# Kernel tuning notes

Measured on AMD Instinct MI355X. Metric: run time of the kernel, lower is better.

The kernel has to match this reference:

```python
import jax, jax.numpy as jnp
import numpy as np


def setup_inputs() -> dict:
    key = jax.random.key(0)
    ks = jax.random.split(key, 6)
    B, C, H, W = 8, 128, 64, 64
    return {
        "curr_features": jax.random.normal(ks[0], (B, C, H, W), jnp.float32),
        "w1": jax.random.normal(ks[1], (C, 2 * C), jnp.float32) * 0.05,   # conv1x1 (2C->C)
        "b1": jnp.zeros((C,), jnp.float32),
        "gamma": jnp.ones((C,), jnp.float32),
        "beta": jnp.zeros((C,), jnp.float32),
        "running_mean": jax.random.normal(ks[2], (C,), jnp.float32) * 0.1,
        "running_var": jax.random.uniform(ks[3], (C,), jnp.float32, 0.5, 1.5),
        "w2": jax.random.normal(ks[4], (1, C), jnp.float32) * 0.05,       # conv1x1 (C->1)
        "b2": jnp.zeros((1,), jnp.float32),
    }


def reference(curr_features, w1, b1, gamma, beta, running_mean, running_var, w2, b2):
    B, C, H, W = curr_features.shape
    M = H * W
    BN_EPS = 1e-5
    LEAKY_SLOPE = 0.01  # InPlaceABNSync default activation: leaky_relu(0.01)

    f = curr_features.reshape(B, C, M)                       # [B,C,M]
    scores = jnp.einsum('bcm,bcn->bmn', f, f) * (C ** -0.5)  # [B,M,M]
    p = jax.nn.softmax(scores, axis=-1)
    feats1 = jnp.einsum('bmn,bcn->bcm', p, f)                # [B,C,M]

    x = jnp.concatenate([feats1, f], axis=1).reshape(B, 2 * C, H, W)

    # cls head: conv1x1 -> BN(inference) -> leaky_relu -> (dropout=identity in eval) -> conv1x1
    y = jnp.einsum('oc,bchw->bohw', w1, x) + b1[None, :, None, None]
    scale = gamma / jnp.sqrt(running_var + BN_EPS)
    y = (y - running_mean[None, :, None, None]) * scale[None, :, None, None] + beta[None, :, None, None]
    y = jnp.where(y >= 0, y, LEAKY_SLOPE * y)
    pred = jnp.einsum('oc,bchw->bohw', w2, y) + b2[None, :, None, None]  # [B,1,H,W]
    return pred
```

## Files before the change

kernel.cpp:

```cpp
#include <hip/hip_runtime.h>

#define NB 8
#define NC 128
#define NM 4096
#define FRAG 512

typedef __attribute__((ext_vector_type(8))) short short8;
typedef __attribute__((ext_vector_type(4))) float floatx4;

#define MFMA(a, b, c) __builtin_amdgcn_mfma_f32_16x16x32_bf16(a, b, c, 0, 0, 0)
#define EXP2F(x) __builtin_amdgcn_exp2f(x)

union S8U { short8 v; uint2 u2[2]; };

__device__ __forceinline__ unsigned pack2bf(float a, float b) {
    unsigned ua = __float_as_uint(a);
    unsigned ub = __float_as_uint(b);
    ua += 0x7fffu + ((ua >> 16) & 1u);
    ub += 0x7fffu + ((ub >> 16) & 1u);
    return (ua >> 16) | (ub & 0xffff0000u);
}

__device__ __forceinline__ unsigned cvt_pk_bf16(float a, float b) {
    unsigned r;
    asm("v_cvt_pk_bf16_f32 %0, %1, %2" : "=v"(r) : "v"(a), "v"(b));
    return r;
}

__constant__ float SF_C = 0.35712442f;
__constant__ float RS_C = 2.8001530f;


__global__ __launch_bounds__(256) void k_prep(
    const float* __restrict__ f, const float* __restrict__ w1,
    unsigned short* __restrict__ fX, unsigned short* __restrict__ gX)
{
    __shared__ __align__(16) char smem[50176];
    float (*Ls)[65] = (float (*)[65])smem;
    unsigned short (*LsT)[132] =
        (unsigned short (*)[132])(smem + 33280);
    unsigned short (*gt2)[72] = (unsigned short (*)[72])smem;

    const int tid   = threadIdx.x;
    const int b     = blockIdx.x & 7;
    const int chunk = blockIdx.x >> 3;
    const int m0    = chunk * 64;
    const float* fb = f + (size_t)b * NC * NM;
    #pragma unroll
    for (int k = 0; k < 32; ++k) {
        int idx = tid + k * 256;
        int c = idx >> 6, mm = idx & 63;
        Ls[c][mm] = fb[(size_t)c * NM + m0 + mm];
    }
    __syncthreads();

    const float sf = SF_C;
    const int m  = tid >> 2;
    const int ks = tid & 3;
    const int ch = ks * 32;
    unsigned pk[16];
    #pragma unroll
    for (int i = 0; i < 16; ++i)
        pk[i] = pack2bf(Ls[ch + 2 * i][m] * sf, Ls[ch + 2 * i + 1][m] * sf);
    {
        const int Mg  = m0 + m;
        const int mt  = Mg >> 4;
        const int lmm = Mg & 15;
        unsigned short* dst = fX + ((size_t)b * 256 + mt) * 4 * FRAG + ks * FRAG;
        #pragma unroll
        for (int q = 0; q < 4; ++q)
            *(uint4*)(dst + (q * 16 + lmm) * 8) =
                make_uint4(pk[4 * q], pk[4 * q + 1], pk[4 * q + 2], pk[4 * q + 3]);
    }
    #pragma unroll
    for (int q = 0; q < 4; ++q)
        *(uint4*)&LsT[m][ks * 32 + q * 8] =
            make_uint4(pk[4 * q], pk[4 * q + 1], pk[4 * q + 2], pk[4 * q + 3]);
    __syncthreads();

    const int wv = tid >> 6;
    const int l  = tid & 63;
    const int lm = l & 15;
    const int lq = l >> 4;
    const float rs = RS_C;

    short8 wf2[2][4];
    #pragma unroll
    for (int j = 0; j < 2; ++j) {
        const int o = (wv * 2 + j) * 16 + lm;
        #pragma unroll
        for (int kk = 0; kk < 4; ++kk) {
            const float* wp = w1 + (size_t)o * (2 * NC) + kk * 32 + lq * 8;
            S8U t;
            t.u2[0] = make_uint2(pack2bf(wp[0] * rs, wp[1] * rs),
                                 pack2bf(wp[2] * rs, wp[3] * rs));
            t.u2[1] = make_uint2(pack2bf(wp[4] * rs, wp[5] * rs),
                                 pack2bf(wp[6] * rs, wp[7] * rs));
            wf2[j][kk] = t.v;
        }
    }
    #pragma unroll
    for (int nt = 0; nt < 4; ++nt) {
        short8 af[4];
        #pragma unroll
        for (int kk = 0; kk < 4; ++kk)
            af[kk] = *(const short8*)&LsT[nt * 16 + lm][kk * 32 + lq * 8];
        #pragma unroll
        for (int j = 0; j < 2; ++j) {
            floatx4 D = {0.f, 0.f, 0.f, 0.f};
            #pragma unroll
            for (int kk = 0; kk < 4; ++kk)
                D = MFMA(af[kk], wf2[j][kk], D);
            *(uint2*)&gt2[(wv * 2 + j) * 16 + lm][nt * 16 + lq * 4] =
                make_uint2(pack2bf(D[0], D[1]), pack2bf(D[2], D[3]));
        }
    }
    __syncthreads();

    const int nblk = chunk >> 1;
    const int k2b  = (chunk & 1) * 2;
    #pragma unroll
    for (int j = 0; j < 2; ++j) {
        const int ot = wv * 2 + j;
        #pragma unroll
        for (int k2l = 0; k2l < 2; ++k2l) {
            uint4 v = *(const uint4*)&gt2[ot * 16 + lm][k2l * 32 + lq * 8];
            *(uint4*)(gX + (((size_t)b * 32 + nblk) * 8 + ot) * 4 * FRAG
                      + (k2b + k2l) * FRAG + l * 8) = v;
        }
    }
}

__global__ __launch_bounds__(256, 2) void k_attn(
    const unsigned short* __restrict__ fX,
    const unsigned short* __restrict__ gX,
    const float* __restrict__ w1,
    const float* __restrict__ b1v, const float* __restrict__ gammav,
    const float* __restrict__ betav, const float* __restrict__ rmeanv,
    const float* __restrict__ rvarv, const float* __restrict__ w2v,
    const float* __restrict__ b2v, float* __restrict__ out)
{
    __shared__ __align__(16) char Ps[2][16384];
    __shared__ float lpart[4][64];
    __shared__ float opart[4][64];

    const int tid = threadIdx.x;
    const int w   = tid >> 6;
    const int l   = tid & 63;
    const int lm  = l & 15;
    const int lq  = l >> 4;
    const int b   = blockIdx.x & 7;
    const int m0  = (blockIdx.x >> 3) * 64;

    const int lq0 = lq & 1;
    const int lq1 = lq >> 1;
    const int lm3 = lm >> 3;
    const unsigned Xsw = (unsigned)(((lq1 << 1) | lm3) << 4);
    const unsigned wofsA =
        ((((unsigned)(w >> 1) * 4 * 16) + ((unsigned)(2 * (w & 1) + lq1) * 16)
          + (unsigned)lm) * 16 + (unsigned)(8 * lq0)) ^ Xsw;
    const unsigned rofs = ((unsigned)l * 16) ^ ((((unsigned)l >> 3) & 3u) << 4);

    const unsigned short* fXb = fX + (size_t)b * NM * NC;
    const unsigned short* gXb = gX + (size_t)b * NC * NM;

    short8 qf[4][4];
    {
        const int qt0 = m0 >> 4;
        #pragma unroll
        for (int mt = 0; mt < 4; ++mt)
            #pragma unroll
            for (int ks = 0; ks < 4; ++ks)
                qf[mt][ks] = *(const short8*)
                    (fXb + (size_t)(qt0 + mt) * 4 * FRAG + ks * FRAG + l * 8);
    }

    const unsigned short* kpA = fXb + (size_t)w * 4 * FRAG + l * 8;
    const unsigned short* kpB = fXb + (size_t)(4 + w) * 4 * FRAG + l * 8;
    const unsigned short* gp0 = gXb + (size_t)(2 * w) * 4 * FRAG + l * 8;
    const unsigned short* gp1 = gXb + (size_t)(2 * w + 1) * 4 * FRAG + l * 8;

    short8 kfA[4], kfB[4];
    short8 gA0[4], gA1[4], gB0[4], gB1[4];
    #pragma unroll
    for (int ks = 0; ks < 4; ++ks) {
        kfA[ks] = *(const short8*)(kpA + ks * FRAG);
        kfB[ks] = *(const short8*)(kpB + ks * FRAG);
    }
    #pragma unroll
    for (int k2 = 0; k2 < 4; ++k2) {
        gA0[k2] = *(const short8*)(gp0 + k2 * FRAG);
        gA1[k2] = *(const short8*)(gp1 + k2 * FRAG);
    }

    floatx4 u[4][2];
    float lsum[4] = {0.f, 0.f, 0.f, 0.f};
    #pragma unroll
    for (int mt = 0; mt < 4; ++mt) {
        u[mt][0] = (floatx4){0.f, 0.f, 0.f, 0.f};
        u[mt][1] = (floatx4){0.f, 0.f, 0.f, 0.f};
    }

    {
        floatx4 svA[4], svB[4];
        __builtin_amdgcn_s_setprio(1);
        #pragma unroll
        for (int mt = 0; mt < 4; ++mt) {
            floatx4 a = {-24.f, -24.f, -24.f, -24.f};
            floatx4 bb = {-24.f, -24.f, -24.f, -24.f};
            #pragma unroll
            for (int ks = 0; ks < 4; ++ks) {
                a  = MFMA(kfA[ks], qf[mt][ks], a);
                bb = MFMA(kfB[ks], qf[mt][ks], bb);
            }
            svA[mt] = a; svB[mt] = bb;
        }
        __builtin_amdgcn_s_setprio(0);
        kpA += 8 * 4 * FRAG; kpB += 8 * 4 * FRAG;
        #pragma unroll
        for (int ks = 0; ks < 4; ++ks) {
            kfA[ks] = *(const short8*)(kpA + ks * FRAG);
            kfB[ks] = *(const short8*)(kpB + ks * FRAG);
        }
        char* psb = Ps[0];
        #pragma unroll
        for (int mt = 0; mt < 4; ++mt) {
            float pA0 = EXP2F(svA[mt][0]);
            float pA1 = EXP2F(svA[mt][1]);
            float pA2 = EXP2F(svA[mt][2]);
            float pA3 = EXP2F(svA[mt][3]);
            float pB0 = EXP2F(svB[mt][0]);
            float pB1 = EXP2F(svB[mt][1]);
            float pB2 = EXP2F(svB[mt][2]);
            float pB3 = EXP2F(svB[mt][3]);
            lsum[mt] += ((pA0 + pA1) + (pA2 + pA3)) +
                        ((pB0 + pB1) + (pB2 + pB3));
            *(uint2*)(psb + mt * 4096 + wofsA) =
                make_uint2(cvt_pk_bf16(pA0, pA1), cvt_pk_bf16(pA2, pA3));
            *(uint2*)(psb + mt * 4096 + wofsA + 2048) =
                make_uint2(cvt_pk_bf16(pB0, pB1), cvt_pk_bf16(pB2, pB3));
        }
        __syncthreads();
    }

    auto body = [&](char* psW, char* psR,
                    short8 (&gC0)[4], short8 (&gC1)[4],
                    short8 (&gN0)[4], short8 (&gN1)[4], bool loadK) {
        floatx4 svA[4], svB[4];
        __builtin_amdgcn_s_setprio(1);
        #pragma unroll
        for (int mt = 0; mt < 4; ++mt) {
            floatx4 a = {-24.f, -24.f, -24.f, -24.f};
            floatx4 bb = {-24.f, -24.f, -24.f, -24.f};
            #pragma unroll
            for (int ks = 0; ks < 4; ++ks) {
                a  = MFMA(kfA[ks], qf[mt][ks], a);
                bb = MFMA(kfB[ks], qf[mt][ks], bb);
            }
            svA[mt] = a; svB[mt] = bb;
        }
        __builtin_amdgcn_s_setprio(0);
        if (loadK) {
            kpA += 8 * 4 * FRAG; kpB += 8 * 4 * FRAG;
            #pragma unroll
            for (int ks = 0; ks < 4; ++ks) {
                kfA[ks] = *(const short8*)(kpA + ks * FRAG);
                kfB[ks] = *(const short8*)(kpB + ks * FRAG);
            }
        }
        gp0 += 8 * 4 * FRAG; gp1 += 8 * 4 * FRAG;
        #pragma unroll
        for (int k2 = 0; k2 < 4; ++k2) {
            gN0[k2] = *(const short8*)(gp0 + k2 * FRAG);
            gN1[k2] = *(const short8*)(gp1 + k2 * FRAG);
        }
        #pragma unroll
        for (int k2 = 0; k2 < 4; ++k2) {
            short8 pf[4];
            #pragma unroll
            for (int mt = 0; mt < 4; ++mt)
                pf[mt] = *(const short8*)(psR + mt * 4096 + k2 * 1024 + rofs);
            __builtin_amdgcn_s_setprio(1);
            #pragma unroll
            for (int mt = 0; mt < 4; ++mt) {
                u[mt][0] = MFMA(pf[mt], gC0[k2], u[mt][0]);
                u[mt][1] = MFMA(pf[mt], gC1[k2], u[mt][1]);
            }
            __builtin_amdgcn_s_setprio(0);
        }
        #pragma unroll
        for (int mt = 0; mt < 4; ++mt) {
            float pA0 = EXP2F(svA[mt][0]);
            float pA1 = EXP2F(svA[mt][1]);
            float pA2 = EXP2F(svA[mt][2]);
            float pA3 = EXP2F(svA[mt][3]);
            float pB0 = EXP2F(svB[mt][0]);
            float pB1 = EXP2F(svB[mt][1]);
            float pB2 = EXP2F(svB[mt][2]);
            float pB3 = EXP2F(svB[mt][3]);
            lsum[mt] += ((pA0 + pA1) + (pA2 + pA3)) +
                        ((pB0 + pB1) + (pB2 + pB3));
            *(uint2*)(psW + mt * 4096 + wofsA) =
                make_uint2(cvt_pk_bf16(pA0, pA1), cvt_pk_bf16(pA2, pA3));
            *(uint2*)(psW + mt * 4096 + wofsA + 2048) =
                make_uint2(cvt_pk_bf16(pB0, pB1), cvt_pk_bf16(pB2, pB3));
        }
        __syncthreads();
    };

    for (int i = 0; i < 15; ++i) {
        body(Ps[1], Ps[0], gA0, gA1, gB0, gB1, true);
        body(Ps[0], Ps[1], gB0, gB1, gA0, gA1, true);
    }
    body(Ps[1], Ps[0], gA0, gA1, gB0, gB1, false);

    #pragma unroll
    for (int k2 = 0; k2 < 4; ++k2) {
        short8 pf[4];
        #pragma unroll
        for (int mt = 0; mt < 4; ++mt)
            pf[mt] = *(const short8*)(Ps[1] + mt * 4096 + k2 * 1024 + rofs);
        __builtin_amdgcn_s_setprio(1);
        #pragma unroll
        for (int mt = 0; mt < 4; ++mt) {
            u[mt][0] = MFMA(pf[mt], gB0[k2], u[mt][0]);
            u[mt][1] = MFMA(pf[mt], gB1[k2], u[mt][1]);
        }
        __builtin_amdgcn_s_setprio(0);
    }

    #pragma unroll
    for (int mt = 0; mt < 4; ++mt) {
        lsum[mt] += __shfl_xor(lsum[mt], 16);
        lsum[mt] += __shfl_xor(lsum[mt], 32);
    }
    if (lq == 0) {
        #pragma unroll
        for (int mt = 0; mt < 4; ++mt)
            lpart[w][mt * 16 + lm] = lsum[mt];
    }

    floatx4 hacc[4][2];
    {
        const float rs = RS_C;
        #pragma unroll
        for (int j = 0; j < 2; ++j) {
            int o = w * 32 + j * 16 + lm;
            short8 wf[4];
            #pragma unroll
            for (int ks = 0; ks < 4; ++ks) {
                const float* wp = w1 + (size_t)o * (2 * NC) + NC + ks * 32 + lq * 8;
                S8U t;
                t.u2[0] = make_uint2(pack2bf(wp[0] * rs, wp[1] * rs),
                                     pack2bf(wp[2] * rs, wp[3] * rs));
                t.u2[1] = make_uint2(pack2bf(wp[4] * rs, wp[5] * rs),
                                     pack2bf(wp[6] * rs, wp[7] * rs));
                wf[ks] = t.v;
            }
            #pragma unroll
            for (int mt = 0; mt < 4; ++mt) {
                floatx4 a = {0.f, 0.f, 0.f, 0.f};
                #pragma unroll
                for (int ks = 0; ks < 4; ++ks)
                    a = MFMA(qf[mt][ks], wf[ks], a);
                hacc[mt][j] = a;
            }
        }
    }
    __syncthreads();

    float Abn[2], Dbn[2], W2[2];
    #pragma unroll
    for (int j = 0; j < 2; ++j) {
        int o = w * 32 + j * 16 + lm;
        float Ar = gammav[o] * rsqrtf(rvarv[o] + 1e-5f);
        Abn[j] = Ar;
        Dbn[j] = (b1v[o] - rmeanv[o]) * Ar + betav[o];
        W2[j]  = w2v[o];
    }
    float av[16];
    #pragma unroll
    for (int mt = 0; mt < 4; ++mt) {
        float4 L0 = *(const float4*)&lpart[0][mt * 16 + lq * 4];
        float4 L1 = *(const float4*)&lpart[1][mt * 16 + lq * 4];
        float4 L2 = *(const float4*)&lpart[2][mt * 16 + lq * 4];
        float4 L3 = *(const float4*)&lpart[3][mt * 16 + lq * 4];
        float4 Lt;
        Lt.x = (L0.x + L1.x) + (L2.x + L3.x);
        Lt.y = (L0.y + L1.y) + (L2.y + L3.y);
        Lt.z = (L0.z + L1.z) + (L2.z + L3.z);
        Lt.w = (L0.w + L1.w) + (L2.w + L3.w);
        #pragma unroll
        for (int r = 0; r < 4; ++r) {
            float rl = 1.f / ((const float*)&Lt)[r];
            float t0 = Abn[0] * (u[mt][0][r] * rl + hacc[mt][0][r]) + Dbn[0];
            float t1 = Abn[1] * (u[mt][1][r] * rl + hacc[mt][1][r]) + Dbn[1];
            t0 = t0 >= 0.f ? t0 : 0.01f * t0;
            t1 = t1 >= 0.f ? t1 : 0.01f * t1;
            av[mt * 4 + r] = W2[0] * t0 + W2[1] * t1;
        }
    }
    #pragma unroll
    for (int i = 0; i < 16; ++i) {
        av[i] += __shfl_xor(av[i], 1);
        av[i] += __shfl_xor(av[i], 2);
        av[i] += __shfl_xor(av[i], 4);
        av[i] += __shfl_xor(av[i], 8);
    }
    if (lm == 0) {
        #pragma unroll
        for (int mt = 0; mt < 4; ++mt)
            #pragma unroll
            for (int r = 0; r < 4; ++r)
                opart[w][mt * 16 + lq * 4 + r] = av[mt * 4 + r];
    }
    __syncthreads();
    if (tid < 64)
        out[(size_t)b * NM + m0 + tid] =
            b2v[0] + opart[0][tid] + opart[1][tid] + opart[2][tid] + opart[3][tid];
}

extern "C" void kernel_launch(void* const* d_in, const int* in_sizes, int n_in,
                              void* d_out, int out_size, void* d_ws, size_t ws_size,
                              hipStream_t stream) {
    const float* f     = (const float*)d_in[0];
    const float* w1    = (const float*)d_in[1];
    const float* b1    = (const float*)d_in[2];
    const float* gamma = (const float*)d_in[3];
    const float* beta  = (const float*)d_in[4];
    const float* rmean = (const float*)d_in[5];
    const float* rvar  = (const float*)d_in[6];
    const float* w2    = (const float*)d_in[7];
    const float* b2    = (const float*)d_in[8];
    float* out = (float*)d_out;

    unsigned short* fX = (unsigned short*)d_ws;
    unsigned short* gX = fX + (size_t)NB * NM * NC;

    hipLaunchKernelGGL(k_prep, dim3(512), dim3(256), 0, stream, f, w1, fX, gX);
    hipLaunchKernelGGL(k_attn, dim3(512), dim3(256), 0, stream,
                       fX, gX, w1, b1, gamma, beta, rmean, rvar, w2, b2, out);
}
```

Before: 159.8 us.

## Split attention over key halves with partial outputs and a merge kernel

Turns the fused attention kernel into a split-K (flash-decoding style) pair: k_attn_p processes half the key range per block across 1024 blocks with a higher occupancy bound, writing unnormalized partial outputs and row sums to workspace. A new k_merge kernel adds the two halves, normalizes, and applies the conv/BN/leaky/conv head. It also reorders the exp/LDS write ahead of the PV MFMA inside the loop body. The aim is more parallelism and occupancy on a 512-block grid; the cost is extra workspace traffic, a third launch, and a fallback path if workspace is too small.

```diff
diff --git a/kernel.cpp b/kernel.cpp
--- a/kernel.cpp
+++ b/kernel.cpp
@@ -29,7 +29,6 @@
 
 __constant__ float SF_C = 0.35712442f;
 __constant__ float RS_C = 2.8001530f;
-
 
 __global__ __launch_bounds__(256) void k_prep(
     const float* __restrict__ f, const float* __restrict__ w1,
@@ -131,26 +130,23 @@
     }
 }
 
-__global__ __launch_bounds__(256, 2) void k_attn(
+__global__ __launch_bounds__(256, 4) void k_attn_p(
     const unsigned short* __restrict__ fX,
     const unsigned short* __restrict__ gX,
-    const float* __restrict__ w1,
-    const float* __restrict__ b1v, const float* __restrict__ gammav,
-    const float* __restrict__ betav, const float* __restrict__ rmeanv,
-    const float* __restrict__ rvarv, const float* __restrict__ w2v,
-    const float* __restrict__ b2v, float* __restrict__ out)
+    float* __restrict__ uP, float* __restrict__ lP)
 {
     __shared__ __align__(16) char Ps[2][16384];
     __shared__ float lpart[4][64];
-    __shared__ float opart[4][64];
 
     const int tid = threadIdx.x;
     const int w   = tid >> 6;
     const int l   = tid & 63;
     const int lm  = l & 15;
     const int lq  = l >> 4;
-    const int b   = blockIdx.x & 7;
-    const int m0  = (blockIdx.x >> 3) * 64;
+    const int s   = blockIdx.x & 511;
+    const int b   = s & 7;
+    const int m0  = ((s >> 3) & 63) * 64;
+    const int nh  = blockIdx.x >> 9;
 
     const int lq0 = lq & 1;
     const int lq1 = lq >> 1;
@@ -175,10 +171,10 @@
                     (fXb + (size_t)(qt0 + mt) * 4 * FRAG + ks * FRAG + l * 8);
     }
 
-    const unsigned short* kpA = fXb + (size_t)w * 4 * FRAG + l * 8;
-    const unsigned short* kpB = fXb + (size_t)(4 + w) * 4 * FRAG + l * 8;
-    const unsigned short* gp0 = gXb + (size_t)(2 * w) * 4 * FRAG + l * 8;
-    const unsigned short* gp1 = gXb + (size_t)(2 * w + 1) * 4 * FRAG + l * 8;
+    const unsigned short* kpA = fXb + (size_t)(nh * 128 + w) * 4 * FRAG + l * 8;
+    const unsigned short* kpB = fXb + (size_t)(nh * 128 + 4 + w) * 4 * FRAG + l * 8;
+    const unsigned short* gp0 = gXb + ((size_t)(nh * 16) * 8 + 2 * w) * 4 * FRAG + l * 8;
+    const unsigned short* gp1 = gp0 + 4 * FRAG;
 
     short8 kfA[4], kfB[4];
     short8 gA0[4], gA1[4], gB0[4], gB1[4];
@@ -275,20 +271,6 @@
             gN1[k2] = *(const short8*)(gp1 + k2 * FRAG);
         }
         #pragma unroll
-        for (int k2 = 0; k2 < 4; ++k2) {
-            short8 pf[4];
-            #pragma unroll
-            for (int mt = 0; mt < 4; ++mt)
-                pf[mt] = *(const short8*)(psR + mt * 4096 + k2 * 1024 + rofs);
-            __builtin_amdgcn_s_setprio(1);
-            #pragma unroll
-            for (int mt = 0; mt < 4; ++mt) {
-                u[mt][0] = MFMA(pf[mt], gC0[k2], u[mt][0]);
-                u[mt][1] = MFMA(pf[mt], gC1[k2], u[mt][1]);
-            }
-            __builtin_amdgcn_s_setprio(0);
-        }
-        #pragma unroll
         for (int mt = 0; mt < 4; ++mt) {
             float pA0 = EXP2F(svA[mt][0]);
             float pA1 = EXP2F(svA[mt][1]);
@@ -305,6 +287,361 @@
             *(uint2*)(psW + mt * 4096 + wofsA + 2048) =
                 make_uint2(cvt_pk_bf16(pB0, pB1), cvt_pk_bf16(pB2, pB3));
         }
+        #pragma unroll
+        for (int k2 = 0; k2 < 4; ++k2) {
+            short8 pf[4];
+            #pragma unroll
+            for (int mt = 0; mt < 4; ++mt)
+                pf[mt] = *(const short8*)(psR + mt * 4096 + k2 * 1024 + rofs);
+            __builtin_amdgcn_s_setprio(1);
+            #pragma unroll
+            for (int mt = 0; mt < 4; ++mt) {
+                u[mt][0] = MFMA(pf[mt], gC0[k2], u[mt][0]);
+                u[mt][1] = MFMA(pf[mt], gC1[k2], u[mt][1]);
+            }
+            __builtin_amdgcn_s_setprio(0);
+        }
+        __syncthreads();
+    };
+
+    for (int i = 0; i < 7; ++i) {
+        body(Ps[1], Ps[0], gA0, gA1, gB0, gB1, true);
+        body(Ps[0], Ps[1], gB0, gB1, gA0, gA1, true);
+    }
+    body(Ps[1], Ps[0], gA0, gA1, gB0, gB1, false);
+
+    #pragma unroll
+    for (int k2 = 0; k2 < 4; ++k2) {
+        short8 pf[4];
+        #pragma unroll
+        for (int mt = 0; mt < 4; ++mt)
+            pf[mt] = *(const short8*)(Ps[1] + mt * 4096 + k2 * 1024 + rofs);
+        __builtin_amdgcn_s_setprio(1);
+        #pragma unroll
+        for (int mt = 0; mt < 4; ++mt) {
+            u[mt][0] = MFMA(pf[mt], gB0[k2], u[mt][0]);
+            u[mt][1] = MFMA(pf[mt], gB1[k2], u[mt][1]);
+        }
+        __builtin_amdgcn_s_setprio(0);
+    }
+
+    #pragma unroll
+    for (int mt = 0; mt < 4; ++mt) {
+        lsum[mt] += __shfl_xor(lsum[mt], 16);
+        lsum[mt] += __shfl_xor(lsum[mt], 32);
+    }
+    if (lq == 0) {
+        #pragma unroll
+        for (int mt = 0; mt < 4; ++mt)
+            lpart[w][mt * 16 + lm] = lsum[mt];
+    }
+    float* ub = uP + ((size_t)s * 2 + nh) * (128 * 64);
+    #pragma unroll
+    for (int mt = 0; mt < 4; ++mt)
+        #pragma unroll
+        for (int j = 0; j < 2; ++j)
+            *(floatx4*)(ub + (size_t)(w * 32 + j * 16 + lm) * 64
+                        + mt * 16 + lq * 4) = u[mt][j];
+    __syncthreads();
+    if (tid < 64)
+        lP[((size_t)s * 2 + nh) * 64 + tid] =
+            lpart[0][tid] + lpart[1][tid] + lpart[2][tid] + lpart[3][tid];
+}
+
+__global__ __launch_bounds__(256) void k_merge(
+    const unsigned short* __restrict__ fX,
+    const float* __restrict__ uP, const float* __restrict__ lP,
+    const float* __restrict__ w1,
+    const float* __restrict__ b1v, const float* __restrict__ gammav,
+    const float* __restrict__ betav, const float* __restrict__ rmeanv,
+    const float* __restrict__ rvarv, const float* __restrict__ w2v,
+    const float* __restrict__ b2v, float* __restrict__ out)
+{
+    __shared__ float opart[4][64];
+    const int tid = threadIdx.x;
+    const int w   = tid >> 6;
+    const int l   = tid & 63;
+    const int lm  = l & 15;
+    const int lq  = l >> 4;
+    const int s   = blockIdx.x;
+    const int b   = s & 7;
+    const int m0  = (s >> 3) * 64;
+
+    const unsigned short* fXb = fX + (size_t)b * NM * NC;
+    short8 qf[4][4];
+    {
+        const int qt0 = m0 >> 4;
+        #pragma unroll
+        for (int mt = 0; mt < 4; ++mt)
+            #pragma unroll
+            for (int ks = 0; ks < 4; ++ks)
+                qf[mt][ks] = *(const short8*)
+                    (fXb + (size_t)(qt0 + mt) * 4 * FRAG + ks * FRAG + l * 8);
+    }
+
+    floatx4 u[4][2];
+    {
+        const float* u0 = uP + ((size_t)s * 2 + 0) * (128 * 64);
+        const float* u1 = uP + ((size_t)s * 2 + 1) * (128 * 64);
+        #pragma unroll
+        for (int mt = 0; mt < 4; ++mt)
+            #pragma unroll
+            for (int j = 0; j < 2; ++j) {
+                size_t ofs = (size_t)(w * 32 + j * 16 + lm) * 64 + mt * 16 + lq * 4;
+                u[mt][j] = *(const floatx4*)(u0 + ofs) + *(const floatx4*)(u1 + ofs);
+            }
+    }
+
+    floatx4 hacc[4][2];
+    {
+        const float rs = RS_C;
+        #pragma unroll
+        for (int j = 0; j < 2; ++j) {
+            int o = w * 32 + j * 16 + lm;
+            short8 wf[4];
+            #pragma unroll
+            for (int ks = 0; ks < 4; ++ks) {
+                const float* wp = w1 + (size_t)o * (2 * NC) + NC + ks * 32 + lq * 8;
+                S8U t;
+                t.u2[0] = make_uint2(pack2bf(wp[0] * rs, wp[1] * rs),
+                                     pack2bf(wp[2] * rs, wp[3] * rs));
+                t.u2[1] = make_uint2(pack2bf(wp[4] * rs, wp[5] * rs),
+                                     pack2bf(wp[6] * rs, wp[7] * rs));
+                wf[ks] = t.v;
+            }
+            #pragma unroll
+            for (int mt = 0; mt < 4; ++mt) {
+                floatx4 a = {0.f, 0.f, 0.f, 0.f};
+                #pragma unroll
+                for (int ks = 0; ks < 4; ++ks)
+                    a = MFMA(qf[mt][ks], wf[ks], a);
+                hacc[mt][j] = a;
+            }
+        }
+    }
+
+    float Abn[2], Dbn[2], W2[2];
+    #pragma unroll
+    for (int j = 0; j < 2; ++j) {
+        int o = w * 32 + j * 16 + lm;
+        float Ar = gammav[o] * rsqrtf(rvarv[o] + 1e-5f);
+        Abn[j] = Ar;
+        Dbn[j] = (b1v[o] - rmeanv[o]) * Ar + betav[o];
+        W2[j]  = w2v[o];
+    }
+    const float* l0 = lP + ((size_t)s * 2 + 0) * 64;
+    const float* l1 = lP + ((size_t)s * 2 + 1) * 64;
+    float av[16];
+    #pragma unroll
+    for (int mt = 0; mt < 4; ++mt) {
+        float4 La = *(const float4*)&l0[mt * 16 + lq * 4];
+        float4 Lb = *(const float4*)&l1[mt * 16 + lq * 4];
+        float4 Lt = make_float4(La.x + Lb.x, La.y + Lb.y,
+                                La.z + Lb.z, La.w + Lb.w);
+        #pragma unroll
+        for (int r = 0; r < 4; ++r) {
+            float rl = 1.f / ((const float*)&Lt)[r];
+            float t0 = Abn[0] * (u[mt][0][r] * rl + hacc[mt][0][r]) + Dbn[0];
+            float t1 = Abn[1] * (u[mt][1][r] * rl + hacc[mt][1][r]) + Dbn[1];
+            t0 = t0 >= 0.f ? t0 : 0.01f * t0;
+            t1 = t1 >= 0.f ? t1 : 0.01f * t1;
+            av[mt * 4 + r] = W2[0] * t0 + W2[1] * t1;
+        }
+    }
+    #pragma unroll
+    for (int i = 0; i < 16; ++i) {
+        av[i] += __shfl_xor(av[i], 1);
+        av[i] += __shfl_xor(av[i], 2);
+        av[i] += __shfl_xor(av[i], 4);
+        av[i] += __shfl_xor(av[i], 8);
+    }
+    if (lm == 0) {
+        #pragma unroll
+        for (int mt = 0; mt < 4; ++mt)
+            #pragma unroll
+            for (int r = 0; r < 4; ++r)
+                opart[w][mt * 16 + lq * 4 + r] = av[mt * 4 + r];
+    }
+    __syncthreads();
+    if (tid < 64)
+        out[(size_t)b * NM + m0 + tid] =
+            b2v[0] + opart[0][tid] + opart[1][tid] + opart[2][tid] + opart[3][tid];
+}
+
+__global__ __launch_bounds__(256, 2) void k_attn(
+    const unsigned short* __restrict__ fX,
+    const unsigned short* __restrict__ gX,
+    const float* __restrict__ w1,
+    const float* __restrict__ b1v, const float* __restrict__ gammav,
+    const float* __restrict__ betav, const float* __restrict__ rmeanv,
+    const float* __restrict__ rvarv, const float* __restrict__ w2v,
+    const float* __restrict__ b2v, float* __restrict__ out)
+{
+    __shared__ __align__(16) char Ps[2][16384];
+    __shared__ float lpart[4][64];
+    __shared__ float opart[4][64];
+
+    const int tid = threadIdx.x;
+    const int w   = tid >> 6;
+    const int l   = tid & 63;
+    const int lm  = l & 15;
+    const int lq  = l >> 4;
+    const int b   = blockIdx.x & 7;
+    const int m0  = (blockIdx.x >> 3) * 64;
+
+    const int lq0 = lq & 1;
+    const int lq1 = lq >> 1;
+    const int lm3 = lm >> 3;
+    const unsigned Xsw = (unsigned)(((lq1 << 1) | lm3) << 4);
+    const unsigned wofsA =
+        ((((unsigned)(w >> 1) * 4 * 16) + ((unsigned)(2 * (w & 1) + lq1) * 16)
+          + (unsigned)lm) * 16 + (unsigned)(8 * lq0)) ^ Xsw;
+    const unsigned rofs = ((unsigned)l * 16) ^ ((((unsigned)l >> 3) & 3u) << 4);
+
+    const unsigned short* fXb = fX + (size_t)b * NM * NC;
+    const unsigned short* gXb = gX + (size_t)b * NC * NM;
+
+    short8 qf[4][4];
+    {
+        const int qt0 = m0 >> 4;
+        #pragma unroll
+        for (int mt = 0; mt < 4; ++mt)
+            #pragma unroll
+            for (int ks = 0; ks < 4; ++ks)
+                qf[mt][ks] = *(const short8*)
+                    (fXb + (size_t)(qt0 + mt) * 4 * FRAG + ks * FRAG + l * 8);
+    }
+
+    const unsigned short* kpA = fXb + (size_t)w * 4 * FRAG + l * 8;
+    const unsigned short* kpB = fXb + (size_t)(4 + w) * 4 * FRAG + l * 8;
+    const unsigned short* gp0 = gXb + (size_t)(2 * w) * 4 * FRAG + l * 8;
+    const unsigned short* gp1 = gXb + (size_t)(2 * w + 1) * 4 * FRAG + l * 8;
+
+    short8 kfA[4], kfB[4];
+    short8 gA0[4], gA1[4], gB0[4], gB1[4];
+    #pragma unroll
+    for (int ks = 0; ks < 4; ++ks) {
+        kfA[ks] = *(const short8*)(kpA + ks * FRAG);
+        kfB[ks] = *(const short8*)(kpB + ks * FRAG);
+    }
+    #pragma unroll
+    for (int k2 = 0; k2 < 4; ++k2) {
+        gA0[k2] = *(const short8*)(gp0 + k2 * FRAG);
+        gA1[k2] = *(const short8*)(gp1 + k2 * FRAG);
+    }
+
+    floatx4 u[4][2];
+    float lsum[4] = {0.f, 0.f, 0.f, 0.f};
+    #pragma unroll
+    for (int mt = 0; mt < 4; ++mt) {
+        u[mt][0] = (floatx4){0.f, 0.f, 0.f, 0.f};
+        u[mt][1] = (floatx4){0.f, 0.f, 0.f, 0.f};
+    }
+
+    {
+        floatx4 svA[4], svB[4];
+        __builtin_amdgcn_s_setprio(1);
+        #pragma unroll
+        for (int mt = 0; mt < 4; ++mt) {
+            floatx4 a = {-24.f, -24.f, -24.f, -24.f};
+            floatx4 bb = {-24.f, -24.f, -24.f, -24.f};
+            #pragma unroll
+            for (int ks = 0; ks < 4; ++ks) {
+                a  = MFMA(kfA[ks], qf[mt][ks], a);
+                bb = MFMA(kfB[ks], qf[mt][ks], bb);
+            }
+            svA[mt] = a; svB[mt] = bb;
+        }
+        __builtin_amdgcn_s_setprio(0);
+        kpA += 8 * 4 * FRAG; kpB += 8 * 4 * FRAG;
+        #pragma unroll
+        for (int ks = 0; ks < 4; ++ks) {
+            kfA[ks] = *(const short8*)(kpA + ks * FRAG);
+            kfB[ks] = *(const short8*)(kpB + ks * FRAG);
+        }
+        char* psb = Ps[0];
+        #pragma unroll
+        for (int mt = 0; mt < 4; ++mt) {
+            float pA0 = EXP2F(svA[mt][0]);
+            float pA1 = EXP2F(svA[mt][1]);
+            float pA2 = EXP2F(svA[mt][2]);
+            float pA3 = EXP2F(svA[mt][3]);
+            float pB0 = EXP2F(svB[mt][0]);
+            float pB1 = EXP2F(svB[mt][1]);
+            float pB2 = EXP2F(svB[mt][2]);
+            float pB3 = EXP2F(svB[mt][3]);
+            lsum[mt] += ((pA0 + pA1) + (pA2 + pA3)) +
+                        ((pB0 + pB1) + (pB2 + pB3));
+            *(uint2*)(psb + mt * 4096 + wofsA) =
+                make_uint2(cvt_pk_bf16(pA0, pA1), cvt_pk_bf16(pA2, pA3));
+            *(uint2*)(psb + mt * 4096 + wofsA + 2048) =
+                make_uint2(cvt_pk_bf16(pB0, pB1), cvt_pk_bf16(pB2, pB3));
+        }
+        __syncthreads();
+    }
+
+    auto body = [&](char* psW, char* psR,
+                    short8 (&gC0)[4], short8 (&gC1)[4],
+                    short8 (&gN0)[4], short8 (&gN1)[4], bool loadK) {
+        floatx4 svA[4], svB[4];
+        __builtin_amdgcn_s_setprio(1);
+        #pragma unroll
+        for (int mt = 0; mt < 4; ++mt) {
+            floatx4 a = {-24.f, -24.f, -24.f, -24.f};
+            floatx4 bb = {-24.f, -24.f, -24.f, -24.f};
+            #pragma unroll
+            for (int ks = 0; ks < 4; ++ks) {
+                a  = MFMA(kfA[ks], qf[mt][ks], a);
+                bb = MFMA(kfB[ks], qf[mt][ks], bb);
+            }
+            svA[mt] = a; svB[mt] = bb;
+        }
+        __builtin_amdgcn_s_setprio(0);
+        if (loadK) {
+            kpA += 8 * 4 * FRAG; kpB += 8 * 4 * FRAG;
+            #pragma unroll
+            for (int ks = 0; ks < 4; ++ks) {
+                kfA[ks] = *(const short8*)(kpA + ks * FRAG);
+                kfB[ks] = *(const short8*)(kpB + ks * FRAG);
+            }
+        }
+        gp0 += 8 * 4 * FRAG; gp1 += 8 * 4 * FRAG;
+        #pragma unroll
+        for (int k2 = 0; k2 < 4; ++k2) {
+            gN0[k2] = *(const short8*)(gp0 + k2 * FRAG);
+            gN1[k2] = *(const short8*)(gp1 + k2 * FRAG);
+        }
+        #pragma unroll
+        for (int mt = 0; mt < 4; ++mt) {
+            float pA0 = EXP2F(svA[mt][0]);
+            float pA1 = EXP2F(svA[mt][1]);
+            float pA2 = EXP2F(svA[mt][2]);
+            float pA3 = EXP2F(svA[mt][3]);
+            float pB0 = EXP2F(svB[mt][0]);
+            float pB1 = EXP2F(svB[mt][1]);
+            float pB2 = EXP2F(svB[mt][2]);
+            float pB3 = EXP2F(svB[mt][3]);
+            lsum[mt] += ((pA0 + pA1) + (pA2 + pA3)) +
+                        ((pB0 + pB1) + (pB2 + pB3));
+            *(uint2*)(psW + mt * 4096 + wofsA) =
+                make_uint2(cvt_pk_bf16(pA0, pA1), cvt_pk_bf16(pA2, pA3));
+            *(uint2*)(psW + mt * 4096 + wofsA + 2048) =
+                make_uint2(cvt_pk_bf16(pB0, pB1), cvt_pk_bf16(pB2, pB3));
+        }
+        #pragma unroll
+        for (int k2 = 0; k2 < 4; ++k2) {
+            short8 pf[4];
+            #pragma unroll
+            for (int mt = 0; mt < 4; ++mt)
+                pf[mt] = *(const short8*)(psR + mt * 4096 + k2 * 1024 + rofs);
+            __builtin_amdgcn_s_setprio(1);
+            #pragma unroll
+            for (int mt = 0; mt < 4; ++mt) {
+                u[mt][0] = MFMA(pf[mt], gC0[k2], u[mt][0]);
+                u[mt][1] = MFMA(pf[mt], gC1[k2], u[mt][1]);
+            }
+            __builtin_amdgcn_s_setprio(0);
+        }
         __syncthreads();
     };
 
@@ -436,8 +773,22 @@
 
     unsigned short* fX = (unsigned short*)d_ws;
     unsigned short* gX = fX + (size_t)NB * NM * NC;
+    float* uP = (float*)(gX + (size_t)NB * NM * NC);
+    float* lP = uP + (size_t)1024 * 128 * 64;
+
+    const size_t ws_needed = (size_t)32 * 1024 * 1024 +
+                             (size_t)1024 * 128 * 64 * 4 +
+                             (size_t)1024 * 64 * 4;
 
     hipLaunchKernelGGL(k_prep, dim3(512), dim3(256), 0, stream, f, w1, fX, gX);
-    hipLaunchKernelGGL(k_attn, dim3(512), dim3(256), 0, stream,
-                       fX, gX, w1, b1, gamma, beta, rmean, rvar, w2, b2, out);
+    if (ws_size >= ws_needed) {
+        hipLaunchKernelGGL(k_attn_p, dim3(1024), dim3(256), 0, stream,
+                           fX, gX, uP, lP);
+        hipLaunchKernelGGL(k_merge, dim3(512), dim3(256), 0, stream,
+                           fX, uP, lP, w1, b1, gamma, beta, rmean, rvar,
+                           w2, b2, out);
+    } else {
+        hipLaunchKernelGGL(k_attn, dim3(512), dim3(256), 0, stream,
+                           fX, gX, w1, b1, gamma, beta, rmean, rvar, w2, b2, out);
+    }
 }
```

Measured after the change: 535.8 us. +235.3%, slower.
